# Performance work log

Measured on AMD Instinct MI355X. Metric: run time of the kernel, lower is better.

Reference implementation:

```python
import jax, jax.numpy as jnp
import numpy as np

LEVELS = 16
FEATURES = 2
HASHMAP_SIZE = 524288  # 2**19
BASE_RES = 16
PER_LEVEL_SCALE = 1.5
N_POINTS = 2097152  # 2**21

# Per-level grid resolutions, computed exactly like the torch code: int(base*scale**l)
_RES = np.array([int(BASE_RES * PER_LEVEL_SCALE ** l) for l in range(LEVELS)], dtype=np.float32)

# Instant-NGP spatial hash primes
_P1, _P2, _P3 = np.int32(73856093), np.int32(19349663), np.int32(83492791)


def setup_inputs() -> dict:
    key = jax.random.key(0)
    k1, k2 = jax.random.split(key)
    x = jax.random.uniform(k1, (N_POINTS, 3), dtype=jnp.float32)
    # Stacked learned hash tables: [L, T, F], init randn*0.01 as in the module
    tables = jax.random.normal(k2, (LEVELS, HASHMAP_SIZE, FEATURES), dtype=jnp.float32) * 0.01
    return {"x": x, "tables": tables}


def reference(x, tables):
    # x: [N, 3] float; tables: [L, T, F] float
    res = jnp.asarray(_RES)                       # [L]
    pos = x[None, :, :] * res[:, None, None]      # [L, N, 3]
    p = jnp.floor(pos).astype(jnp.int32)          # [L, N, 3] (matches torch .int())
    # Spatial hash with int32 wrap-around, identical to torch int32 semantics
    h = (p[..., 0] * _P1) ^ (p[..., 1] * _P2) ^ (p[..., 2] * _P3)
    idx = jnp.mod(h, np.int32(HASHMAP_SIZE))      # [L, N], nonnegative (sign of divisor)
    emb = jax.vmap(lambda t, i: t[i])(tables, idx)  # [L, N, F] per-level gather
    n = x.shape[0]
    # concat over levels along last dim -> [N, L*F]
    return jnp.transpose(emb, (1, 0, 2)).reshape(n, LEVELS * FEATURES)
```

## Files before the change

### kernel.cpp

```cpp
#include <hip/hip_runtime.h>

#define LEVELS 16
#define TSIZE 524288
#define TMASK (TSIZE - 1)
#define TPB 256
#define GPPT 8
#define CHUNK (TPB * GPPT)

typedef float f2v __attribute__((ext_vector_type(2)));
typedef float f4v __attribute__((ext_vector_type(4)));

__device__ __constant__ float c_res[LEVELS] = {
    16.f, 24.f, 36.f, 54.f, 81.f, 121.f, 182.f, 273.f,
    410.f, 615.f, 922.f, 1383.f, 2075.f, 3113.f, 4670.f, 7006.f
};

__device__ __forceinline__ unsigned hash_idx(float px, float py, float pz, float r)
{
    const int ix = (int)floorf(px * r);
    const int iy = (int)floorf(py * r);
    const int iz = (int)floorf(pz * r);
    const unsigned h = (unsigned)ix * 73856093u
                     ^ (unsigned)iy * 19349663u
                     ^ (unsigned)iz * 83492791u;
    return h & TMASK;
}


__global__ __launch_bounds__(TPB) void gather_kernel(
    const float* __restrict__ x,
    const float* __restrict__ tables,
    f2v* __restrict__ ws,
    int n, int bpl)
{
    const int b = blockIdx.x;
    const int half = b / (8 * bpl);
    const int r = b % (8 * bpl);
    const int level = half * 8 + (r & 7);
    const int c = r >> 3;
    const int t = threadIdx.x;

    const float rs = c_res[level];
    const float* __restrict__ tbl = tables + (size_t)level * (TSIZE * 2);
    f2v* __restrict__ slab = ws + ((size_t)c * LEVELS + level) * CHUNK;
    const long long base = (long long)c * CHUNK;

    if (base + CHUNK <= n) {
        const float* __restrict__ xb = x + 3 * base;

        float px[GPPT], py[GPPT], pz[GPPT];
#pragma unroll
        for (int j = 0; j < GPPT; ++j) {
            const int local = j * TPB + t;
            px[j] = xb[3 * local + 0];
            py[j] = xb[3 * local + 1];
            pz[j] = xb[3 * local + 2];
        }

        unsigned idx[GPPT];
#pragma unroll
        for (int j = 0; j < GPPT; ++j)
            idx[j] = hash_idx(px[j], py[j], pz[j], rs);

        f2v e[GPPT];
#pragma unroll
        for (int j = 0; j < GPPT; ++j)
            e[j] = *reinterpret_cast<const f2v*>(tbl + 2 * (size_t)idx[j]);

#pragma unroll
        for (int j = 0; j < GPPT; ++j)
            __builtin_nontemporal_store(e[j], slab + j * TPB + t);
    } else {
#pragma unroll
        for (int j = 0; j < GPPT; ++j) {
            const int local = j * TPB + t;
            const long long p = base + local;
            if (p < n) {
                const float qx = x[3 * p + 0];
                const float qy = x[3 * p + 1];
                const float qz = x[3 * p + 2];
                const unsigned idx = hash_idx(qx, qy, qz, rs);
                const f2v e = *reinterpret_cast<const f2v*>(tbl + 2 * (size_t)idx);
                __builtin_nontemporal_store(e, slab + local);
            }
        }
    }
}

__global__ __launch_bounds__(TPB) void assemble_kernel(
    const f2v* __restrict__ ws,
    float* __restrict__ out,
    int n)
{
    const int c = blockIdx.x;
    const int t = threadIdx.x;
    const int q = t & 7;
    const int sub = t >> 3;

    const f2v* __restrict__ wa = ws + ((size_t)c * LEVELS + 2 * q) * CHUNK;
    const f2v* __restrict__ wb = wa + CHUNK;
    const long long base = (long long)c * CHUNK;

    if (base + CHUNK <= n) {
#pragma unroll 8
        for (int u = 0; u < CHUNK / 64; ++u) {
            const int lp = 2 * (u * 32 + sub);
            const f4v a = __builtin_nontemporal_load(
                reinterpret_cast<const f4v*>(wa + lp));
            const f4v b = __builtin_nontemporal_load(
                reinterpret_cast<const f4v*>(wb + lp));
            f4v v0, v1;
            v0.x = a.x; v0.y = a.y; v0.z = b.x; v0.w = b.y;
            v1.x = a.z; v1.y = a.w; v1.z = b.z; v1.w = b.w;
            float* row = out + (size_t)(base + lp) * (2 * LEVELS) + 4 * q;
            __builtin_nontemporal_store(v0, reinterpret_cast<f4v*>(row));
            __builtin_nontemporal_store(v1, reinterpret_cast<f4v*>(row + 2 * LEVELS));
        }
    } else {
#pragma unroll 8
        for (int u = 0; u < CHUNK / 32; ++u) {
            const int lp = u * 32 + sub;
            const long long pt = base + lp;
            if (pt < n) {
                const f2v a = __builtin_nontemporal_load(wa + lp);
                const f2v b = __builtin_nontemporal_load(wb + lp);
                f4v v;
                v.x = a.x; v.y = a.y; v.z = b.x; v.w = b.y;
                __builtin_nontemporal_store(
                    v, reinterpret_cast<f4v*>(out + (size_t)pt * (2 * LEVELS) + 4 * q));
            }
        }
    }
}

#define ROWW 34
__global__ __launch_bounds__(TPB) void hashgrid_fused(
    const float* __restrict__ x,
    const float* __restrict__ tables,
    float* __restrict__ out,
    int n)
{
    __shared__ float lds[TPB * ROWW];
    const int t = threadIdx.x;

    for (long long base = (long long)blockIdx.x * TPB; base < n;
         base += (long long)gridDim.x * TPB) {
        const int p = (int)base + t;
        float px = 0.f, py = 0.f, pz = 0.f;
        if (p < n) {
            px = x[3 * (size_t)p + 0];
            py = x[3 * (size_t)p + 1];
            pz = x[3 * (size_t)p + 2];
        }
#pragma unroll
        for (int l = 0; l < LEVELS; ++l) {
            if (p < n) {
                const unsigned idx = hash_idx(px, py, pz, c_res[l]);
                const f2v e = *reinterpret_cast<const f2v*>(
                    tables + (((size_t)l * TSIZE + idx) << 1));
                *reinterpret_cast<f2v*>(lds + t * ROWW + 2 * l) = e;
            }
            __syncthreads();
        }
#pragma unroll
        for (int it = 0; it < 8; ++it) {
            const int lp = it * 32 + (t >> 3);
            const int qq = t & 7;
            const int gp = (int)base + lp;
            if (gp < n) {
                const f2v a = *reinterpret_cast<const f2v*>(lds + lp * ROWW + 4 * qq);
                const f2v b = *reinterpret_cast<const f2v*>(lds + lp * ROWW + 4 * qq + 2);
                f4v v;
                v.x = a.x; v.y = a.y; v.z = b.x; v.w = b.y;
                __builtin_nontemporal_store(
                    v, reinterpret_cast<f4v*>(out + (size_t)gp * (2 * LEVELS) + 4 * qq));
            }
        }
        __syncthreads();
    }
}

extern "C" void kernel_launch(void* const* d_in, const int* in_sizes, int n_in,
                              void* d_out, int out_size, void* d_ws, size_t ws_size,
                              hipStream_t stream)
{
    const float* x      = (const float*)d_in[0];
    const float* tables = (const float*)d_in[1];
    float* out          = (float*)d_out;
    const int n = in_sizes[0] / 3;

    const int bpl = (n + CHUNK - 1) / CHUNK;
    const size_t ws_need = (size_t)bpl * LEVELS * CHUNK * sizeof(f2v);
    if (ws_size < ws_need) {
        int grid = 1024;
        const int nblocks = (n + TPB - 1) / TPB;
        if (nblocks < grid) grid = nblocks;
        hashgrid_fused<<<grid, TPB, 0, stream>>>(x, tables, out, n);
        return;
    }

    f2v* ws = (f2v*)d_ws;
    gather_kernel<<<2 * 8 * bpl, TPB, 0, stream>>>(x, tables, ws, n, bpl);
    assemble_kernel<<<bpl, TPB, 0, stream>>>(ws, out, n);
}
```

Baseline: 333.3 us.

## Fuse gather and assemble kernels via per-chunk atomic counters and spin-wait

Merges the two-kernel gather/assemble pipeline into one launch. Each block finishes its per-level gather, atomically bumps a per-chunk counter, and the blocks handling the second half of the levels spin until all 16 levels of their chunk are done, then each assembles one eighth of that chunk into the output. The aim is to remove the second kernel launch and its grid-wide barrier so assembly can overlap with gathering. In exchange it adds a memset, atomics and busy-waiting that rely on the waited-for blocks being scheduled; deadlock is avoided only because those blocks have lower block ids. It also assumes the relaxed spin plus barrier gives visibility of the other blocks' workspace writes.

Result: slower. 1.011 ms (+203.4%).

```diff
diff --git a/kernel.cpp b/kernel.cpp
--- a/kernel.cpp
+++ b/kernel.cpp
@@ -26,17 +26,19 @@
     return h & TMASK;
 }
 
-
-__global__ __launch_bounds__(TPB) void gather_kernel(
+__global__ __launch_bounds__(TPB) void fused_gather_assemble(
     const float* __restrict__ x,
     const float* __restrict__ tables,
+    unsigned* __restrict__ cnt,
     f2v* __restrict__ ws,
+    float* __restrict__ out,
     int n, int bpl)
 {
     const int b = blockIdx.x;
     const int half = b / (8 * bpl);
     const int r = b % (8 * bpl);
-    const int level = half * 8 + (r & 7);
+    const int q = r & 7;
+    const int level = half * 8 + q;
     const int c = r >> 3;
     const int t = threadIdx.x;
 
@@ -85,49 +87,54 @@
             }
         }
     }
-}
-
-__global__ __launch_bounds__(TPB) void assemble_kernel(
-    const f2v* __restrict__ ws,
-    float* __restrict__ out,
-    int n)
-{
-    const int c = blockIdx.x;
-    const int t = threadIdx.x;
-    const int q = t & 7;
+
+    __syncthreads();
+    if (t == 0)
+        __hip_atomic_fetch_add(&cnt[c], 1u, __ATOMIC_RELEASE,
+                               __HIP_MEMORY_SCOPE_AGENT);
+
+    if (half == 0) return;
+
+    if (t == 0) {
+        while (__hip_atomic_load(&cnt[c], __ATOMIC_RELAXED,
+                                 __HIP_MEMORY_SCOPE_AGENT) < (unsigned)LEVELS)
+            __builtin_amdgcn_s_sleep(8);
+    }
+    __syncthreads();
+
+    const int qq = t & 7;
     const int sub = t >> 3;
-
-    const f2v* __restrict__ wa = ws + ((size_t)c * LEVELS + 2 * q) * CHUNK;
+    const f2v* __restrict__ wa = ws + ((size_t)c * LEVELS + 2 * qq) * CHUNK;
     const f2v* __restrict__ wb = wa + CHUNK;
-    const long long base = (long long)c * CHUNK;
+    const int sb = q * (CHUNK / 8);
 
     if (base + CHUNK <= n) {
-#pragma unroll 8
-        for (int u = 0; u < CHUNK / 64; ++u) {
-            const int lp = 2 * (u * 32 + sub);
+#pragma unroll
+        for (int u = 0; u < CHUNK / 8 / 64; ++u) {
+            const int lp = sb + 2 * (u * 32 + sub);
             const f4v a = __builtin_nontemporal_load(
                 reinterpret_cast<const f4v*>(wa + lp));
-            const f4v b = __builtin_nontemporal_load(
+            const f4v bb = __builtin_nontemporal_load(
                 reinterpret_cast<const f4v*>(wb + lp));
             f4v v0, v1;
-            v0.x = a.x; v0.y = a.y; v0.z = b.x; v0.w = b.y;
-            v1.x = a.z; v1.y = a.w; v1.z = b.z; v1.w = b.w;
-            float* row = out + (size_t)(base + lp) * (2 * LEVELS) + 4 * q;
+            v0.x = a.x; v0.y = a.y; v0.z = bb.x; v0.w = bb.y;
+            v1.x = a.z; v1.y = a.w; v1.z = bb.z; v1.w = bb.w;
+            float* row = out + (size_t)(base + lp) * (2 * LEVELS) + 4 * qq;
             __builtin_nontemporal_store(v0, reinterpret_cast<f4v*>(row));
             __builtin_nontemporal_store(v1, reinterpret_cast<f4v*>(row + 2 * LEVELS));
         }
     } else {
-#pragma unroll 8
-        for (int u = 0; u < CHUNK / 32; ++u) {
-            const int lp = u * 32 + sub;
+#pragma unroll
+        for (int u = 0; u < CHUNK / 8 / 32; ++u) {
+            const int lp = sb + u * 32 + sub;
             const long long pt = base + lp;
             if (pt < n) {
                 const f2v a = __builtin_nontemporal_load(wa + lp);
-                const f2v b = __builtin_nontemporal_load(wb + lp);
+                const f2v bb = __builtin_nontemporal_load(wb + lp);
                 f4v v;
-                v.x = a.x; v.y = a.y; v.z = b.x; v.w = b.y;
+                v.x = a.x; v.y = a.y; v.z = bb.x; v.w = bb.y;
                 __builtin_nontemporal_store(
-                    v, reinterpret_cast<f4v*>(out + (size_t)pt * (2 * LEVELS) + 4 * q));
+                    v, reinterpret_cast<f4v*>(out + (size_t)pt * (2 * LEVELS) + 4 * qq));
             }
         }
     }
@@ -190,7 +197,8 @@
     const int n = in_sizes[0] / 3;
 
     const int bpl = (n + CHUNK - 1) / CHUNK;
-    const size_t ws_need = (size_t)bpl * LEVELS * CHUNK * sizeof(f2v);
+    const size_t cnt_bytes = ((size_t)bpl * sizeof(unsigned) + 255) & ~(size_t)255;
+    const size_t ws_need = cnt_bytes + (size_t)bpl * LEVELS * CHUNK * sizeof(f2v);
     if (ws_size < ws_need) {
         int grid = 1024;
         const int nblocks = (n + TPB - 1) / TPB;
@@ -199,7 +207,10 @@
         return;
     }
 
-    f2v* ws = (f2v*)d_ws;
-    gather_kernel<<<2 * 8 * bpl, TPB, 0, stream>>>(x, tables, ws, n, bpl);
-    assemble_kernel<<<bpl, TPB, 0, stream>>>(ws, out, n);
-}
+    unsigned* cnt = (unsigned*)d_ws;
+    f2v* ws = (f2v*)((char*)d_ws + cnt_bytes);
+
+    hipMemsetAsync(d_ws, 0, cnt_bytes, stream);
+    fused_gather_assemble<<<2 * 8 * bpl, TPB, 0, stream>>>(
+        x, tables, cnt, ws, out, n, bpl);
+}
```
